# Optimization experiments

Measured on AMD Instinct MI355X. Metric: run time of the kernel, lower is better.

## Reference

```python
import jax, jax.numpy as jnp
import numpy as np

B, S, D, H = 4, 2048, 2048, 16
HD = D // H            # 128 head dim
HID = 5632             # SwiGLU hidden: multiple_of*ceil((2/3*4*D)/multiple_of)
EPS = 1e-6


def setup_inputs() -> dict:
    key = jax.random.key(0)
    ks = jax.random.split(key, 12)
    s = 0.02
    x = jax.random.normal(ks[0], (B, S, D), dtype=jnp.float32)
    # RoPE freqs (theta=10000), complex freqs_cis represented as cos/sin
    inv_freq = 1.0 / (10000.0 ** (np.arange(0, HD, 2, dtype=np.float32) / HD))
    t = np.arange(S, dtype=np.float32)
    ang = np.outer(t, inv_freq)                      # [S, HD/2]
    freqs_cos = jnp.asarray(np.cos(ang), dtype=jnp.float32)
    freqs_sin = jnp.asarray(np.sin(ang), dtype=jnp.float32)
    # additive causal mask [1,1,S,S]
    mask = jnp.where(jnp.triu(jnp.ones((S, S), dtype=bool), k=1), -jnp.inf, 0.0)
    mask = mask.astype(jnp.float32)[None, None]
    return {
        "x": x,
        "freqs_cos": freqs_cos,
        "freqs_sin": freqs_sin,
        "mask": mask,
        "wq": jax.random.normal(ks[1], (D, D), jnp.float32) * s,
        "wk": jax.random.normal(ks[2], (D, D), jnp.float32) * s,
        "wv": jax.random.normal(ks[3], (D, D), jnp.float32) * s,
        "wo": jax.random.normal(ks[4], (D, D), jnp.float32) * s,
        "w1": jax.random.normal(ks[5], (HID, D), jnp.float32) * s,
        "w2": jax.random.normal(ks[6], (D, HID), jnp.float32) * s,
        "w3": jax.random.normal(ks[7], (HID, D), jnp.float32) * s,
        "attn_norm_w": jnp.ones((D,), jnp.float32),
        "ffn_norm_w": jnp.ones((D,), jnp.float32),
        "start_pos": 0,
    }


def rmsnorm(x, w, eps=EPS):
    xf = x.astype(jnp.float32)
    y = xf * jax.lax.rsqrt(jnp.mean(xf * xf, axis=-1, keepdims=True) + eps)
    return y.astype(x.dtype) * w


def apply_rope(q, k, cos, sin):
    # q,k: [B,S,H,HD]; cos,sin: [S,HD/2]
    def rot(x):
        xf = x.astype(jnp.float32).reshape(*x.shape[:-1], HD // 2, 2)
        xr, xi = xf[..., 0], xf[..., 1]
        c = cos[None, :, None, :]
        s = sin[None, :, None, :]
        out = jnp.stack([xr * c - xi * s, xr * s + xi * c], axis=-1)
        return out.reshape(*x.shape).astype(x.dtype)
    return rot(q), rot(k)


def reference(x, freqs_cos, freqs_sin, mask, wq, wk, wv, wo, w1, w2, w3,
              attn_norm_w, ffn_norm_w, start_pos):
    # ---- attention ----
    xa = rmsnorm(x, attn_norm_w)
    q = (xa @ wq.T).reshape(B, S, H, HD)
    k = (xa @ wk.T).reshape(B, S, H, HD)
    v = (xa @ wv.T).reshape(B, S, H, HD)
    q, k = apply_rope(q, k, freqs_cos, freqs_sin)
    # [B,H,S,S] scores (naive, materialized as in original)
    scores = jnp.einsum('bqhd,bkhd->bhqk', q, k) / jnp.sqrt(jnp.float32(HD))
    scores = scores + mask
    attn = jax.nn.softmax(scores, axis=-1)
    o = jnp.einsum('bhqk,bkhd->bqhd', attn, v).reshape(B, S, D)
    h = x + o @ wo.T
    # ---- SwiGLU FFN ----
    hf = rmsnorm(h, ffn_norm_w)
    ff = (jax.nn.silu(hf @ w1.T) * (hf @ w3.T)) @ w2.T
    return h + ff
```

## Files before the change

kernel.cpp:

```cpp
#include <hip/hip_runtime.h>
#include <hip/hip_bf16.h>
#include <stdint.h>

typedef short  bf16x8_t __attribute__((ext_vector_type(8)));
typedef short  bf16x4_t __attribute__((ext_vector_type(4)));
typedef float  f32x4_t  __attribute__((ext_vector_type(4)));
typedef unsigned short u16;
typedef unsigned int   u32;

#define DEV __device__ __forceinline__

DEV u16 f2bf(float f){
  u32 u = __float_as_uint(f);
  u += 0x7fffu + ((u >> 16) & 1u);
  return (u16)(u >> 16);
}
DEV float bf2f(u16 h){ return __uint_as_float(((u32)h) << 16); }

DEV void gl16(const void* g, void* l){
  __builtin_amdgcn_global_load_lds(
      (const __attribute__((address_space(1))) void*)g,
      (__attribute__((address_space(3))) void*)l, 16, 0, 0);
}

#define BAR() __builtin_amdgcn_s_barrier()
#define WL8() asm volatile("s_waitcnt lgkmcnt(8)" ::: "memory")
#define WL0() asm volatile("s_waitcnt lgkmcnt(0)" ::: "memory")

__global__ __launch_bounds__(256) void cvt_k(const float* __restrict__ in,
                                             u16* __restrict__ out, int n8){
  int i = blockIdx.x * 256 + threadIdx.x;
  if (i >= n8) return;
  const float4* p = (const float4*)in;
  float4 a = p[(size_t)i*2], b = p[(size_t)i*2+1];
  bf16x8_t o;
  o[0]=(short)f2bf(a.x); o[1]=(short)f2bf(a.y); o[2]=(short)f2bf(a.z); o[3]=(short)f2bf(a.w);
  o[4]=(short)f2bf(b.x); o[5]=(short)f2bf(b.y); o[6]=(short)f2bf(b.z); o[7]=(short)f2bf(b.w);
  *(bf16x8_t*)(out + (size_t)i*8) = o;
}

__global__ __launch_bounds__(256) void rmsnorm_k(const float* __restrict__ x,
                                                 const float* __restrict__ w,
                                                 u16* __restrict__ y){
  int row = blockIdx.x, t = threadIdx.x;
  const float4* xr = (const float4*)(x + (size_t)row*2048);
  float4 a = xr[t*2], b = xr[t*2+1];
  float ss = a.x*a.x+a.y*a.y+a.z*a.z+a.w*a.w + b.x*b.x+b.y*b.y+b.z*b.z+b.w*b.w;
  #pragma unroll
  for (int m = 32; m; m >>= 1) ss += __shfl_xor(ss, m, 64);
  __shared__ float red[4];
  if ((t & 63) == 0) red[t >> 6] = ss;
  __syncthreads();
  float tot = red[0]+red[1]+red[2]+red[3];
  float rs = rsqrtf(tot * (1.0f/2048.0f) + 1e-6f);
  const float4* wr = (const float4*)w;
  float4 wa = wr[t*2], wb = wr[t*2+1];
  bf16x8_t o;
  o[0]=(short)f2bf(a.x*rs*wa.x); o[1]=(short)f2bf(a.y*rs*wa.y);
  o[2]=(short)f2bf(a.z*rs*wa.z); o[3]=(short)f2bf(a.w*rs*wa.w);
  o[4]=(short)f2bf(b.x*rs*wb.x); o[5]=(short)f2bf(b.y*rs*wb.y);
  o[6]=(short)f2bf(b.z*rs*wb.z); o[7]=(short)f2bf(b.w*rs*wb.w);
  *(bf16x8_t*)(y + (size_t)row*2048 + t*8) = o;
}

__global__ __launch_bounds__(256) void rmsnorm2_k(const float* __restrict__ x,
                                                  const u16* __restrict__ t1,
                                                  const float* __restrict__ w,
                                                  u16* __restrict__ y){
  int row = blockIdx.x, t = threadIdx.x;
  const float4* xr = (const float4*)(x + (size_t)row*2048);
  float4 a = xr[t*2], b = xr[t*2+1];
  bf16x8_t tv = *(const bf16x8_t*)(t1 + (size_t)row*2048 + t*8);
  float h[8];
  h[0]=a.x+bf2f((u16)tv[0]); h[1]=a.y+bf2f((u16)tv[1]);
  h[2]=a.z+bf2f((u16)tv[2]); h[3]=a.w+bf2f((u16)tv[3]);
  h[4]=b.x+bf2f((u16)tv[4]); h[5]=b.y+bf2f((u16)tv[5]);
  h[6]=b.z+bf2f((u16)tv[6]); h[7]=b.w+bf2f((u16)tv[7]);
  float ss = 0.f;
  #pragma unroll
  for (int j=0;j<8;j++) ss += h[j]*h[j];
  #pragma unroll
  for (int m = 32; m; m >>= 1) ss += __shfl_xor(ss, m, 64);
  __shared__ float red[4];
  if ((t & 63) == 0) red[t >> 6] = ss;
  __syncthreads();
  float tot = red[0]+red[1]+red[2]+red[3];
  float rs = rsqrtf(tot * (1.0f/2048.0f) + 1e-6f);
  const float4* wr = (const float4*)w;
  float4 wa = wr[t*2], wb = wr[t*2+1];
  bf16x8_t o;
  o[0]=(short)f2bf(h[0]*rs*wa.x); o[1]=(short)f2bf(h[1]*rs*wa.y);
  o[2]=(short)f2bf(h[2]*rs*wa.z); o[3]=(short)f2bf(h[3]*rs*wa.w);
  o[4]=(short)f2bf(h[4]*rs*wb.x); o[5]=(short)f2bf(h[5]*rs*wb.y);
  o[6]=(short)f2bf(h[6]*rs*wb.z); o[7]=(short)f2bf(h[7]*rs*wb.w);
  *(bf16x8_t*)(y + (size_t)row*2048 + t*8) = o;
}

__global__ __launch_bounds__(256) void rope_k(u16* __restrict__ q, u16* __restrict__ k,
                                              const float* __restrict__ fc,
                                              const float* __restrict__ fs){
  int i = blockIdx.x * 256 + threadIdx.x;
  int ii = i & 63; int h = (i >> 6) & 15; int bs = i >> 10;
  int s = bs & 2047;
  size_t off = (size_t)bs*2048 + h*128 + 2*ii;
  float c = fc[s*64+ii], sn = fs[s*64+ii];
  u32 qq = *(u32*)(q + off);
  float xr = bf2f((u16)(qq & 0xffff)), xi = bf2f((u16)(qq >> 16));
  *(u32*)(q + off) = (u32)f2bf(xr*c - xi*sn) | ((u32)f2bf(xr*sn + xi*c) << 16);
  u32 kk = *(u32*)(k + off);
  xr = bf2f((u16)(kk & 0xffff)); xi = bf2f((u16)(kk >> 16));
  *(u32*)(k + off) = (u32)f2bf(xr*c - xi*sn) | ((u32)f2bf(xr*sn + xi*c) << 16);
}

__global__ __launch_bounds__(256) void transpose_k(const u16* __restrict__ in,
                                                   u16* __restrict__ out){
  __shared__ u16 tile[64*68];
  int tid = threadIdx.x;
  int tm = blockIdx.x >> 5, tn = blockIdx.x & 31;
  const u16* src = in + (size_t)(tm*64)*2048 + tn*64;
  #pragma unroll
  for (int i=0;i<2;i++){
    int idx = i*256 + tid;
    int r = idx >> 3, c8 = (idx & 7)*8;
    *(bf16x8_t*)&tile[r*68 + c8] = *(const bf16x8_t*)(src + (size_t)r*2048 + c8);
  }
  __syncthreads();
  u16* dst = out + (size_t)(tn*64)*8192 + tm*64;
  #pragma unroll
  for (int i=0;i<2;i++){
    int idx = i*256 + tid;
    int oc = idx >> 3, r8 = (idx & 7)*8;
    bf16x8_t v;
    #pragma unroll
    for (int j=0;j<8;j++) v[j] = tile[(r8+j)*68 + oc];
    *(bf16x8_t*)(dst + (size_t)oc*8192 + r8) = v;
  }
}


#define RA(BUF,MH) { \
  Ar[0][0]=*(const bf16x8_t*)(pA +BUF*16384+MH*4096);      \
  Ar[0][1]=*(const bf16x8_t*)(pAx+BUF*16384+MH*4096);      \
  Ar[1][0]=*(const bf16x8_t*)(pA +BUF*16384+MH*4096+1024); \
  Ar[1][1]=*(const bf16x8_t*)(pAx+BUF*16384+MH*4096+1024); \
  Ar[2][0]=*(const bf16x8_t*)(pA +BUF*16384+MH*4096+2048); \
  Ar[2][1]=*(const bf16x8_t*)(pAx+BUF*16384+MH*4096+2048); \
  Ar[3][0]=*(const bf16x8_t*)(pA +BUF*16384+MH*4096+3072); \
  Ar[3][1]=*(const bf16x8_t*)(pAx+BUF*16384+MH*4096+3072); }
#define RB(DST,BUF,NHL) { \
  DST[0][0]=*(const bf16x8_t*)(pB +BUF*16384+NHL*2048);      \
  DST[0][1]=*(const bf16x8_t*)(pBx+BUF*16384+NHL*2048);      \
  DST[1][0]=*(const bf16x8_t*)(pB +BUF*16384+NHL*2048+1024); \
  DST[1][1]=*(const bf16x8_t*)(pBx+BUF*16384+NHL*2048+1024); }
#define STG_A(BUF,HALF,COL) { \
  gl16(gA + (COL) + HALF*K128,       dA + BUF*16384 + HALF*8192); \
  gl16(gA + (COL) + HALF*K128 + K64, dA + BUF*16384 + HALF*8192 + 4096); }
#define STG_B(BUF,HALF,COL) { \
  gl16(gB + (COL) + HALF*K128,       dB + BUF*16384 + HALF*8192); \
  gl16(gB + (COL) + HALF*K128 + K64, dB + BUF*16384 + HALF*8192 + 4096); }

DEV void MMQ(bf16x8_t (&a)[4][2], bf16x8_t (&b)[2][2], int mh, int nhl,
             f32x4_t (&acc)[8][4]){
  __builtin_amdgcn_s_setprio(1);
  #pragma unroll
  for (int kk=0;kk<2;kk++)
    #pragma unroll
    for (int mi=0;mi<4;mi++)
      #pragma unroll
      for (int nj=0;nj<2;nj++)
        acc[mh*4+mi][nhl*2+nj] = __builtin_amdgcn_mfma_f32_16x16x32_bf16(
            a[mi][kk], b[nj][kk], acc[mh*4+mi][nhl*2+nj], 0,0,0);
  __builtin_amdgcn_s_setprio(0);
}

template<int EPI>
__global__ __launch_bounds__(512, 2) void gemm_bt(const u16* __restrict__ A,
                                                  const u16* __restrict__ B,
                                                  void* __restrict__ C,
                                                  const void* __restrict__ aux,
                                                  const void* __restrict__ aux2,
                                                  int M, int N, int K){
  __shared__ __align__(16) u16 sA[2][2][8192];
  __shared__ __align__(16) u16 sB[2][2][8192];
  int tid = threadIdx.x, lane = tid & 63, wave = tid >> 6;
  int l15 = lane & 15, l4 = lane >> 4;
  int nbn = N / 256;
  int nwg = gridDim.x, bid = blockIdx.x;
  int qq = nwg >> 3, rr = nwg & 7;
  int xc = bid & 7, yy = bid >> 3;
  int wg = (xc < rr ? xc*(qq+1) : rr*(qq+1) + (xc-rr)*qq) + yy;
  int tm = wg / nbn, tn = wg % nbn;
  size_t m0 = (size_t)tm*256, n0 = (size_t)tn*256;
  const u16* Ag = A + m0*K;
  const u16* Bg = B + n0*K;
  int wm = wave >> 2, wn = wave & 3;
  int bh = wn >> 1, wn1 = wn & 1;

  int ch0 = l4 ^ (l15 & 7);
  const u16* pA  = &sA[0][wm][l15*64 + ch0*8];
  const u16* pAx = &sA[0][wm][l15*64 + (ch0^4)*8];
  const u16* pB  = &sB[0][bh][(wn1*64 + l15)*64 + ch0*8];
  const u16* pBx = &sB[0][bh][(wn1*64 + l15)*64 + (ch0^4)*8];
  int r0 = tid >> 3;
  int lg = (tid & 7) ^ (r0 & 7);
  const u16* gA = Ag + (size_t)r0*K + lg*8;
  const u16* gB = Bg + (size_t)r0*K + lg*8;
  size_t K64 = (size_t)K*64, K128 = K64*2;
  u16* dA = &sA[0][0][tid*8];
  u16* dB = &sB[0][0][tid*8];

  f32x4_t acc[8][4];
  #pragma unroll
  for (int i=0;i<8;i++)
    #pragma unroll
    for (int j=0;j<4;j++)
      acc[i][j] = (f32x4_t){0.f,0.f,0.f,0.f};
  bf16x8_t Ar[4][2], Br0[2][2], Br1[2][2];
  int nk = K / 64;

  STG_A(0,0,0); STG_A(0,1,0);
  STG_B(0,0,0); STG_B(0,1,0);
  STG_B(1,0,(size_t)64); STG_B(1,1,(size_t)64);
  asm volatile("s_waitcnt vmcnt(4)" ::: "memory");
  BAR();

  for (int i=0; i<nk/2; ++i){
    int T0 = 2*i;
    bool s2 = (T0+2 < nk), s3 = (T0+3 < nk);
    size_t c1 = (size_t)(T0+1)*64, c2 = (size_t)(T0+2)*64, c3 = (size_t)(T0+3)*64;
    RA(0,0); RB(Br0,0,0);
    STG_A(1,0,c1);
    WL8(); BAR(); WL0();
    MMQ(Ar, Br0, 0, 0, acc);
    BAR();
    RB(Br1,0,1);
    STG_A(1,1,c1);
    BAR(); WL0();
    MMQ(Ar, Br1, 0, 1, acc);
    BAR();
    RA(0,1);
    if (s2) STG_B(0,0,c2);
    BAR(); WL0();
    MMQ(Ar, Br0, 1, 0, acc);
    BAR();
    if (s2){
      STG_B(0,1,c2);
      asm volatile("s_waitcnt vmcnt(4)" ::: "memory");
    } else {
      asm volatile("s_waitcnt vmcnt(0)" ::: "memory");
    }
    BAR(); WL0();
    MMQ(Ar, Br1, 1, 1, acc);
    BAR();
    RA(1,0); RB(Br0,1,0);
    if (s2) STG_A(0,0,c2);
    WL8(); BAR(); WL0();
    MMQ(Ar, Br0, 0, 0, acc);
    BAR();
    RB(Br1,1,1);
    if (s2) STG_A(0,1,c2);
    BAR(); WL0();
    MMQ(Ar, Br1, 0, 1, acc);
    BAR();
    RA(1,1);
    if (s3) STG_B(1,0,c3);
    BAR(); WL0();
    MMQ(Ar, Br0, 1, 0, acc);
    BAR();
    if (s3){
      STG_B(1,1,c3);
      asm volatile("s_waitcnt vmcnt(4)" ::: "memory");
    } else {
      asm volatile("s_waitcnt vmcnt(0)" ::: "memory");
    }
    BAR(); WL0();
    MMQ(Ar, Br1, 1, 1, acc);
    BAR();
  }

  #pragma unroll
  for (int am=0; am<8; am++)
    #pragma unroll
    for (int ni=0; ni<4; ni++)
      #pragma unroll
      for (int r=0; r<4; r++){
        float v = acc[am][ni][r];
        size_t rowg = m0 + (am&3)*16 + (am>>2)*64 + wm*128 + l4*4 + r;
        size_t colg = n0 + wn*64 + ni*16 + l15;
        size_t idx = rowg * (size_t)N + colg;
        if constexpr (EPI == 0){
          ((u16*)C)[idx] = f2bf(v);
        } else if constexpr (EPI == 1){
          float s = v / (1.0f + __expf(-v));
          ((u16*)C)[idx] = f2bf(s);
        } else if constexpr (EPI == 2){
          float a = bf2f(((const u16*)aux)[idx]);
          ((u16*)C)[idx] = f2bf(v * a);
        } else {
          float a = ((const float*)aux)[idx];
          float b2 = bf2f(((const u16*)aux2)[idx]);
          ((float*)C)[idx] = v + a + b2;
        }
      }
}

__global__ __launch_bounds__(256) void attn_k(const u16* __restrict__ Q,
                                              const u16* __restrict__ K,
                                              const u16* __restrict__ VT,
                                              u16* __restrict__ O){
  __shared__ __align__(16) u16 sK[32*128];
  __shared__ __align__(16) u16 sVT[128*32];
  int tid = threadIdx.x, lane = tid & 63, wave = tid >> 6;
  int bid = blockIdx.x;
  int qt = 31 - (bid >> 6);
  int bh = bid & 63; int b = bh >> 4, h = bh & 15;
  int l15 = lane & 15, l4 = lane >> 4;
  size_t base = ((size_t)b*2048)*2048 + (size_t)h*128;
  const u16* VTg0 = VT + ((size_t)h*128)*8192 + (size_t)b*2048;
  int qr0 = qt*64 + wave*16;
  int qrow = qr0 + l15;
  bf16x8_t qf[4];
  #pragma unroll
  for (int s=0;s<4;s++)
    qf[s] = *(const bf16x8_t*)(Q + base + (size_t)qrow*2048 + s*32 + l4*8);

  f32x4_t oaccT[8];
  #pragma unroll
  for (int f=0;f<8;f++) oaccT[f] = (f32x4_t){0.f,0.f,0.f,0.f};
  float lrun = 0.f;

  const float cl2 = 0.08838834764831845f * 1.4426950408889634f;
  int nkt = (qt + 1) * 2;
  for (int kt=0; kt<nkt; ++kt){
    __syncthreads();
    const u16* Kg = K + base + (size_t)kt*32*2048;
    #pragma unroll
    for (int i=0;i<2;i++){
      int c = i*256 + tid; int row = c>>4;
      gl16(Kg + (size_t)row*2048 + (size_t)(((c&15) ^ (row&7))*8), &sK[c*8]);
    }
    #pragma unroll
    for (int i=0;i<2;i++){
      int c = i*256 + tid; int d = c>>2;
      gl16(VTg0 + (size_t)d*8192 + kt*32 + (size_t)((((c&3) ^ ((d>>1)&3)))*8),
           &sVT[c*8]);
    }
    __syncthreads();

    if (kt*32 <= qr0 + 15){
      f32x4_t sacc[2];
      sacc[0] = (f32x4_t){0.f,0.f,0.f,0.f};
      sacc[1] = (f32x4_t){0.f,0.f,0.f,0.f};
      __builtin_amdgcn_s_setprio(1);
      #pragma unroll
      for (int n=0;n<2;n++)
        #pragma unroll
        for (int s=0;s<4;s++){
          bf16x8_t kf = *(const bf16x8_t*)
              &sK[(n*16 + l15)*128 + (((s*4 + l4) ^ (l15 & 7))*8)];
          sacc[n] = __builtin_amdgcn_mfma_f32_16x16x32_bf16(kf, qf[s], sacc[n], 0,0,0);
        }
      __builtin_amdgcn_s_setprio(0);
      float sum = 0.f;
      bf16x8_t pa;
      bool diag = (kt*32 + 31 > qr0);
      if (diag){
        #pragma unroll
        for (int j=0;j<8;j++){
          int n = j>>2, r = j&3;
          float p = exp2f(sacc[n][r] * cl2);
          int kg = kt*32 + n*16 + l4*4 + r;
          if (kg > qrow) p = 0.f;
          sum += p;
          pa[j] = (short)f2bf(p);
        }
      } else {
        #pragma unroll
        for (int j=0;j<8;j++){
          float p = exp2f(sacc[j>>2][j&3] * cl2);
          sum += p;
          pa[j] = (short)f2bf(p);
        }
      }
      sum += __shfl_xor(sum, 16, 64);
      sum += __shfl_xor(sum, 32, 64);
      lrun += sum;
      __builtin_amdgcn_s_setprio(1);
      #pragma unroll
      for (int f=0;f<8;f++){
        int d = f*16 + l15;
        bf16x4_t lo = *(const bf16x4_t*)&sVT[d*32 + (((0*4 + l4) ^ (d & 6))*4)];
        bf16x4_t hi = *(const bf16x4_t*)&sVT[d*32 + (((1*4 + l4) ^ (d & 6))*4)];
        bf16x8_t va;
        va[0]=lo[0]; va[1]=lo[1]; va[2]=lo[2]; va[3]=lo[3];
        va[4]=hi[0]; va[5]=hi[1]; va[6]=hi[2]; va[7]=hi[3];
        oaccT[f] = __builtin_amdgcn_mfma_f32_16x16x32_bf16(va, pa, oaccT[f], 0,0,0);
      }
      __builtin_amdgcn_s_setprio(0);
    }
  }
  float inv = 1.0f / lrun;
  size_t orow = (size_t)b*2048 + qrow;
  #pragma unroll
  for (int f=0;f<8;f++){
    bf16x4_t ov;
    ov[0]=(short)f2bf(oaccT[f][0]*inv); ov[1]=(short)f2bf(oaccT[f][1]*inv);
    ov[2]=(short)f2bf(oaccT[f][2]*inv); ov[3]=(short)f2bf(oaccT[f][3]*inv);
    *(bf16x4_t*)(O + orow*2048 + h*128 + f*16 + l4*4) = ov;
  }
}

extern "C" void kernel_launch(void* const* d_in, const int* in_sizes, int n_in,
                              void* d_out, int out_size, void* d_ws, size_t ws_size,
                              hipStream_t stream){
  (void)in_sizes; (void)n_in; (void)out_size; (void)ws_size;
  const float* x   = (const float*)d_in[0];
  const float* fc  = (const float*)d_in[1];
  const float* fs  = (const float*)d_in[2];
  const float* wq  = (const float*)d_in[4];
  const float* wk  = (const float*)d_in[5];
  const float* wv  = (const float*)d_in[6];
  const float* wo  = (const float*)d_in[7];
  const float* w1  = (const float*)d_in[8];
  const float* w2  = (const float*)d_in[9];
  const float* w3  = (const float*)d_in[10];
  const float* anw = (const float*)d_in[11];
  const float* fnw = (const float*)d_in[12];
  float* out = (float*)d_out;
  char* ws = (char*)d_ws;

  const int M = 8192, D = 2048, HID = 5632;
  const size_t WB   = 23068672ull;
  const size_t ACT2 = 33554432ull;

  u16* wbuf = (u16*)(ws);
  u16* xa   = (u16*)(ws + WB);
  u16* qb   = (u16*)(ws + WB + ACT2);
  u16* kb   = (u16*)(ws + WB + 2*ACT2);
  u16* vb   = (u16*)(ws + WB + 3*ACT2);
  u16* g1   = (u16*)(ws + WB + 4*ACT2);
  u16* vt = g1;
  u16* t1 = qb;
  u16* hf = kb;

  rmsnorm_k<<<M, 256, 0, stream>>>(x, anw, xa);

  cvt_k<<<D*D/8/256, 256, 0, stream>>>(wq, wbuf, D*D/8);
  gemm_bt<0><<<(M/256)*(D/256), 512, 0, stream>>>(xa, wbuf, qb, nullptr, nullptr, M, D, D);
  cvt_k<<<D*D/8/256, 256, 0, stream>>>(wk, wbuf, D*D/8);
  gemm_bt<0><<<(M/256)*(D/256), 512, 0, stream>>>(xa, wbuf, kb, nullptr, nullptr, M, D, D);
  cvt_k<<<D*D/8/256, 256, 0, stream>>>(wv, wbuf, D*D/8);
  gemm_bt<0><<<(M/256)*(D/256), 512, 0, stream>>>(xa, wbuf, vb, nullptr, nullptr, M, D, D);

  rope_k<<<32768, 256, 0, stream>>>(qb, kb, fc, fs);
  transpose_k<<<4096, 256, 0, stream>>>(vb, vt);

  attn_k<<<2048, 256, 0, stream>>>(qb, kb, vt, xa);

  cvt_k<<<D*D/8/256, 256, 0, stream>>>(wo, wbuf, D*D/8);
  gemm_bt<0><<<(M/256)*(D/256), 512, 0, stream>>>(xa, wbuf, t1, nullptr, nullptr, M, D, D);

  rmsnorm2_k<<<M, 256, 0, stream>>>(x, t1, fnw, hf);

  cvt_k<<<HID*D/8/256, 256, 0, stream>>>(w1, wbuf, HID*D/8);
  gemm_bt<1><<<(M/256)*(HID/256), 512, 0, stream>>>(hf, wbuf, g1, nullptr, nullptr, M, HID, D);
  cvt_k<<<HID*D/8/256, 256, 0, stream>>>(w3, wbuf, HID*D/8);
  gemm_bt<2><<<(M/256)*(HID/256), 512, 0, stream>>>(hf, wbuf, g1, g1, nullptr, M, HID, D);
  cvt_k<<<HID*D/8/256, 256, 0, stream>>>(w2, wbuf, HID*D/8);
  gemm_bt<4><<<(M/256)*(D/256), 512, 0, stream>>>(g1, wbuf, out, x, t1, M, D, HID);
}
```

Measured before the change: 1.117 ms.

## Fuse QKV projections into one GEMM and double-buffer attention K/V loads

The three Q/K/V projection GEMMs are merged into a single GEMM over a concatenated 6144-row weight buffer. A new epilogue routes each output column block to the q, k or v buffer, which removes two launches and improves wave occupancy across the grid. The attention kernel now double-buffers its K and V^T tiles in LDS and prefetches tile kt+2 while tile kt is computed, using vmcnt waits. This hides global load latency at the cost of twice the LDS per block, which may reduce occupancy, and it requires a larger weight workspace.

Measured after the change: 1.124 ms. Within noise of the previous version (+0.6%).

```diff
diff --git a/kernel.cpp b/kernel.cpp
--- a/kernel.cpp
+++ b/kernel.cpp
@@ -296,10 +296,14 @@
         } else if constexpr (EPI == 2){
           float a = bf2f(((const u16*)aux)[idx]);
           ((u16*)C)[idx] = f2bf(v * a);
-        } else {
+        } else if constexpr (EPI == 4){
           float a = ((const float*)aux)[idx];
           float b2 = bf2f(((const u16*)aux2)[idx]);
           ((float*)C)[idx] = v + a + b2;
+        } else {
+          int mat = (int)(colg >> 11);
+          u16* dst = (mat==0) ? (u16*)C : (mat==1) ? (u16*)aux : (u16*)aux2;
+          dst[rowg*2048 + (colg & 2047)] = f2bf(v);
         }
       }
 }
@@ -308,8 +312,8 @@
                                               const u16* __restrict__ K,
                                               const u16* __restrict__ VT,
                                               u16* __restrict__ O){
-  __shared__ __align__(16) u16 sK[32*128];
-  __shared__ __align__(16) u16 sVT[128*32];
+  __shared__ __align__(16) u16 sK[2][32*128];
+  __shared__ __align__(16) u16 sVT[2][128*32];
   int tid = threadIdx.x, lane = tid & 63, wave = tid >> 6;
   int bid = blockIdx.x;
   int qt = 31 - (bid >> 6);
@@ -331,22 +335,30 @@
 
   const float cl2 = 0.08838834764831845f * 1.4426950408889634f;
   int nkt = (qt + 1) * 2;
-  for (int kt=0; kt<nkt; ++kt){
-    __syncthreads();
-    const u16* Kg = K + base + (size_t)kt*32*2048;
+
+  auto STG = [&](int t, int buf){
+    const u16* Kg = K + base + (size_t)t*32*2048;
     #pragma unroll
     for (int i=0;i<2;i++){
       int c = i*256 + tid; int row = c>>4;
-      gl16(Kg + (size_t)row*2048 + (size_t)(((c&15) ^ (row&7))*8), &sK[c*8]);
+      gl16(Kg + (size_t)row*2048 + (size_t)(((c&15) ^ (row&7))*8), &sK[buf][c*8]);
     }
     #pragma unroll
     for (int i=0;i<2;i++){
       int c = i*256 + tid; int d = c>>2;
-      gl16(VTg0 + (size_t)d*8192 + kt*32 + (size_t)((((c&3) ^ ((d>>1)&3)))*8),
-           &sVT[c*8]);
+      gl16(VTg0 + (size_t)d*8192 + t*32 + (size_t)((((c&3) ^ ((d>>1)&3)))*8),
+           &sVT[buf][c*8]);
     }
-    __syncthreads();
-
+  };
+
+  STG(0, 0);
+  STG(1, 1);
+
+  for (int kt=0; kt<nkt; ++kt){
+    if (kt < nkt-1) asm volatile("s_waitcnt vmcnt(4)" ::: "memory");
+    else            asm volatile("s_waitcnt vmcnt(0)" ::: "memory");
+    BAR();
+    int buf = kt & 1;
     if (kt*32 <= qr0 + 15){
       f32x4_t sacc[2];
       sacc[0] = (f32x4_t){0.f,0.f,0.f,0.f};
@@ -357,7 +369,7 @@
         #pragma unroll
         for (int s=0;s<4;s++){
           bf16x8_t kf = *(const bf16x8_t*)
-              &sK[(n*16 + l15)*128 + (((s*4 + l4) ^ (l15 & 7))*8)];
+              &sK[buf][(n*16 + l15)*128 + (((s*4 + l4) ^ (l15 & 7))*8)];
           sacc[n] = __builtin_amdgcn_mfma_f32_16x16x32_bf16(kf, qf[s], sacc[n], 0,0,0);
         }
       __builtin_amdgcn_s_setprio(0);
@@ -389,8 +401,8 @@
       #pragma unroll
       for (int f=0;f<8;f++){
         int d = f*16 + l15;
-        bf16x4_t lo = *(const bf16x4_t*)&sVT[d*32 + (((0*4 + l4) ^ (d & 6))*4)];
-        bf16x4_t hi = *(const bf16x4_t*)&sVT[d*32 + (((1*4 + l4) ^ (d & 6))*4)];
+        bf16x4_t lo = *(const bf16x4_t*)&sVT[buf][d*32 + (((0*4 + l4) ^ (d & 6))*4)];
+        bf16x4_t hi = *(const bf16x4_t*)&sVT[buf][d*32 + (((1*4 + l4) ^ (d & 6))*4)];
         bf16x8_t va;
         va[0]=lo[0]; va[1]=lo[1]; va[2]=lo[2]; va[3]=lo[3];
         va[4]=hi[0]; va[5]=hi[1]; va[6]=hi[2]; va[7]=hi[3];
@@ -398,6 +410,8 @@
       }
       __builtin_amdgcn_s_setprio(0);
     }
+    BAR();
+    if (kt+2 < nkt) STG(kt+2, buf);
   }
   float inv = 1.0f / lrun;
   size_t orow = (size_t)b*2048 + qrow;
@@ -430,7 +444,7 @@
   char* ws = (char*)d_ws;
 
   const int M = 8192, D = 2048, HID = 5632;
-  const size_t WB   = 23068672ull;
+  const size_t WB   = 25165824ull;
   const size_t ACT2 = 33554432ull;
 
   u16* wbuf = (u16*)(ws);
@@ -445,12 +459,10 @@
 
   rmsnorm_k<<<M, 256, 0, stream>>>(x, anw, xa);
 
-  cvt_k<<<D*D/8/256, 256, 0, stream>>>(wq, wbuf, D*D/8);
-  gemm_bt<0><<<(M/256)*(D/256), 512, 0, stream>>>(xa, wbuf, qb, nullptr, nullptr, M, D, D);
-  cvt_k<<<D*D/8/256, 256, 0, stream>>>(wk, wbuf, D*D/8);
-  gemm_bt<0><<<(M/256)*(D/256), 512, 0, stream>>>(xa, wbuf, kb, nullptr, nullptr, M, D, D);
-  cvt_k<<<D*D/8/256, 256, 0, stream>>>(wv, wbuf, D*D/8);
-  gemm_bt<0><<<(M/256)*(D/256), 512, 0, stream>>>(xa, wbuf, vb, nullptr, nullptr, M, D, D);
+  cvt_k<<<D*D/8/256, 256, 0, stream>>>(wq, wbuf,            D*D/8);
+  cvt_k<<<D*D/8/256, 256, 0, stream>>>(wk, wbuf +   D*D,    D*D/8);
+  cvt_k<<<D*D/8/256, 256, 0, stream>>>(wv, wbuf + 2*D*D,    D*D/8);
+  gemm_bt<6><<<(M/256)*(6144/256), 512, 0, stream>>>(xa, wbuf, qb, kb, vb, M, 6144, D);
 
   rope_k<<<32768, 256, 0, stream>>>(qb, kb, fc, fs);
   transpose_k<<<4096, 256, 0, stream>>>(vb, vt);
```
